# Kernel tuning notes

Hardware: AMD Instinct MI355X
Metric: run time of the kernel (lower is better)

Reference implementation:

```python
import jax, jax.numpy as jnp
import numpy as np
import itertools

B, NM, NS, K, HID, NLAYER, MAXZ, OUT = 64, 32, 32, 3, 64, 4, 100, 1
S = B * NS
NREAL = NM - 2  # real nodes per graph (rest padded)


def setup_inputs() -> dict:
    key = jax.random.key(0)
    ks = jax.random.split(key, 12)
    x = jax.random.randint(ks[0], (B, NM, 1), 0, MAXZ + 1, dtype=jnp.int32)
    subadj = jax.random.uniform(ks[1], (B, NM, NM), dtype=jnp.float32)
    # K distinct node ids per subgraph, all within the real (non-padded) nodes
    subgs = jnp.argsort(jax.random.uniform(ks[2], (S, NREAL)), axis=1)[:, :K].astype(jnp.int32)
    num_node = jnp.full((B,), NREAL, dtype=jnp.int32)
    num_subg = jnp.full((B,), NS, dtype=jnp.int32)
    sc = 0.05
    idemb = jax.random.normal(ks[3], (K + 2, HID), jnp.float32) * sc
    node_emb = jax.random.normal(ks[4], (MAXZ + 1, HID), jnp.float32) * sc
    mlp_W1 = jax.random.normal(ks[5], (NLAYER, HID, HID), jnp.float32) * sc
    mlp_b1 = jnp.zeros((NLAYER, HID), jnp.float32)
    mlp_W2 = jax.random.normal(ks[6], (NLAYER, HID, HID), jnp.float32) * sc
    mlp_b2 = jnp.zeros((NLAYER, HID), jnp.float32)
    mlp_g = jnp.ones((NLAYER, HID), jnp.float32)
    mlp_be = jnp.zeros((NLAYER, HID), jnp.float32)
    set1_W = jax.random.normal(ks[7], (HID, HID), jnp.float32) * sc
    set1_b = jnp.zeros((HID,), jnp.float32)
    set2_W = jax.random.normal(ks[8], (HID, HID), jnp.float32) * sc
    set2_b = jnp.zeros((HID,), jnp.float32)
    out_W = jax.random.normal(ks[9], (HID, OUT), jnp.float32) * sc
    out_b = jnp.zeros((OUT,), jnp.float32)
    return dict(x=x, subadj=subadj, subgs=subgs, num_node=num_node, num_subg=num_subg,
                idemb=idemb, node_emb=node_emb, mlp_W1=mlp_W1, mlp_b1=mlp_b1,
                mlp_W2=mlp_W2, mlp_b2=mlp_b2, mlp_g=mlp_g, mlp_be=mlp_be,
                set1_W=set1_W, set1_b=set1_b, set2_W=set2_W, set2_b=set2_b,
                out_W=out_W, out_b=out_b)


def _layernorm(z, g, b):
    m = z.mean(-1, keepdims=True)
    v = ((z - m) ** 2).mean(-1, keepdims=True)
    return (z - m) / jnp.sqrt(v + 1e-5) * g + b


def _forward(x, subadj, subgs, num_node,
             idemb, node_emb, mlp_W1, mlp_b1, mlp_W2, mlp_b2, mlp_g, mlp_be,
             set1_W, set1_b, set2_W, set2_b, out_W, out_b):
    # allperm: (K, K!) -- matches registered buffer extracttuple(arange(k),k).t()
    allperm = jnp.asarray(np.array(list(itertools.permutations(range(K))), dtype=np.int32).T)
    P = allperm.shape[1]  # K! permutations
    subgbatch = jnp.repeat(jnp.arange(B), NS)                       # (S,) graph id of each subgraph
    null_mask = jnp.arange(NM)[None, :] >= num_node[:, None]        # (B, NM) padded-node mask
    h = node_emb[x[..., 0]]                                         # (B, NM, HID) inmlp embedding
    h = jnp.broadcast_to(h[subgbatch][:, :, None, :], (S, NM, P, HID))  # gather per subgraph, expand perms
    # CSR scatter-assign of permutation id embeddings (all rows full size K, distinct nodes)
    labelbatch = jnp.repeat(jnp.arange(S), K)                       # (S*K,)
    labelnodes = subgs.reshape(-1)                                  # (S*K,)
    nodeidx = jnp.tile(jnp.arange(K), S)                            # position within subgraph
    emb = idemb[allperm[nodeidx]]                                   # (S*K, P, HID)
    h = h.at[labelbatch, labelnodes].multiply(emb)                  # unique (subg,node) pairs
    A = subadj[subgbatch]                                           # (S, NM, NM), float path (d=1 broadcast)
    for l in range(NLAYER):
        m = jnp.einsum('bij,bjpd->bipd', A, h)                      # noindexbmm
        m = jax.nn.relu(m @ mlp_W1[l] + mlp_b1[l])
        m = m @ mlp_W2[l] + mlp_b2[l]
        m = jax.nn.relu(_layernorm(m, mlp_g[l], mlp_be[l]))
        h = h + m
    h = jnp.where(null_mask[subgbatch][:, :, None, None], 0.0, h)   # zero padded nodes
    h = jax.nn.relu(h.mean(axis=2) @ set1_W + set1_b)               # setmlp1 over perm-mean: (S, NM, HID)
    h = jax.nn.relu(h.sum(axis=1) @ set2_W + set2_b)                # setmlp2 over node-sum: (S, HID)
    pooled = jax.ops.segment_max(h, subgbatch, num_segments=B)      # global_max_pool: (B, HID)
    return pooled @ out_W + out_b                                   # (B, OUT)


def reference(x, subadj, subgs, num_node, num_subg,
              idemb, node_emb, mlp_W1, mlp_b1, mlp_W2, mlp_b2, mlp_g, mlp_be,
              set1_W, set1_b, set2_W, set2_b, out_W, out_b):
    return _forward(x, subadj, subgs, num_node,
                    idemb, node_emb, mlp_W1, mlp_b1, mlp_W2, mlp_b2, mlp_g, mlp_be,
                    set1_W, set1_b, set2_W, set2_b, out_W, out_b)
```

## Files before the change

### kernel.cpp

```cpp
#include <hip/hip_runtime.h>
#include <math.h>


#define NBATCH 64
#define NM 32
#define NS 32
#define KSUB 3
#define HID 64
#define NLAYER 4
#define PP 6

#define W1F 0
#define W2F 16384
#define S1F 32768
#define GMAX_BYTE 73728
#define CNT_BYTE  90112
#define S2WT_BYTE 90368

#define SH 68
#define SG 36
#define WBU 2304

typedef _Float16 f16x8 __attribute__((ext_vector_type(8)));
typedef _Float16 f16x2 __attribute__((ext_vector_type(2)));
typedef __fp16 fp16x2 __attribute__((ext_vector_type(2)));
typedef float f32x4 __attribute__((ext_vector_type(4)));

#define MFMA16(a, b, c) __builtin_amdgcn_mfma_f32_16x16x32_f16(a, b, c, 0, 0, 0)

__constant__ int c_perm[KSUB][PP] = {
    {0, 0, 1, 1, 2, 2},
    {1, 2, 0, 2, 0, 1},
    {2, 1, 2, 0, 1, 0}
};

__device__ __forceinline__ unsigned pk2rtz(float a, float b) {
    union { fp16x2 h; unsigned u; } x;
    x.h = __builtin_amdgcn_cvt_pkrtz(a, b);
    return x.u;
}
__device__ __forceinline__ uint2 pk4rtz(float a, float b, float c, float d) {
    return make_uint2(pk2rtz(a, b), pk2rtz(c, d));
}
__device__ __forceinline__ unsigned pkadd(unsigned hu, unsigned yu) {
    union { f16x2 h; unsigned u; } a, b;
    a.u = hu; b.u = yu;
    a.h = a.h + b.h;
    return a.u;
}
__device__ __forceinline__ f16x8 frd(const unsigned short* p) {
    union { struct { uint2 a, b; } u; f16x8 f; } x;
    x.u.a = *(const uint2*)p;
    x.u.b = *(const uint2*)(p + 4);
    return x.f;
}
__device__ __forceinline__ f16x8 gfrd(const unsigned short* p) {
    union { uint4 u; f16x8 f; } x;
    x.u = *(const uint4*)p;
    return x.f;
}

extern "C" __global__ void idmpnn_prep(const float* __restrict__ w1,
                                       const float* __restrict__ w2,
                                       const float* __restrict__ s1w,
                                       const float* __restrict__ s2w,
                                       char* __restrict__ ws)
{
    unsigned short* wsu = (unsigned short*)ws;
    int idx = blockIdx.x * 256 + threadIdx.x;
    float v; int dst;
    if (idx < 16384) {
        int l = idx >> 12, r = idx & 4095, dp = r >> 6, e = r & 63;
        v = w1[l * 4096 + e * 64 + dp];
        dst = W1F + idx;
    } else if (idx < 32768) {
        int k = idx - 16384;
        int l = k >> 12, r = k & 4095, dp = r >> 6, e = r & 63;
        v = w2[l * 4096 + e * 64 + dp];
        dst = W2F + k;
    } else if (idx < 36864) {
        int k = idx - 32768, dp = k >> 6, e = k & 63;
        v = s1w[e * 64 + dp];
        dst = S1F + k;
    } else if (idx < 40960) {
        int k = idx - 36864, dp = k >> 6, e = k & 63;
        ((float*)(ws + S2WT_BYTE))[k] = s2w[e * 64 + dp];
        return;
    } else if (idx < 45056) {
        ((unsigned*)(ws + GMAX_BYTE))[idx - 40960] = 0u;
        return;
    } else if (idx < 45120) {
        ((unsigned*)(ws + CNT_BYTE))[idx - 45056] = 0u;
        return;
    } else return;
    union { _Float16 h; unsigned short u; } cv;
    cv.h = (_Float16)v;
    wsu[dst] = cv.u;
}

extern "C" __global__ void __launch_bounds__(384, 2)
idmpnn_main(const int* __restrict__ xg, const float* __restrict__ subadj,
            const int* __restrict__ subgs, const int* __restrict__ num_node,
            const float* __restrict__ idemb, const float* __restrict__ node_emb,
            const float* __restrict__ b1g, const float* __restrict__ b2g,
            const float* __restrict__ lngm, const float* __restrict__ lnbm,
            const float* __restrict__ s1bm, const float* __restrict__ s2bm,
            const float* __restrict__ outw, const float* __restrict__ outb,
            const unsigned short* __restrict__ wsf, const float* __restrict__ s2wt,
            unsigned* __restrict__ gmax, unsigned* __restrict__ cnt,
            float* __restrict__ out)
{
    __shared__ unsigned short WB[12 * WBU];
    __shared__ float idS[KSUB * 64];
    __shared__ float prm[NLAYER * 4 * 64];
    __shared__ float HSf[2 * HID];

    const int s0 = blockIdx.x * 2;
    const int b = s0 >> 5;
    const int tid = threadIdx.x;
    const int w = tid / 64, lane = tid & 63;
    const int c = lane & 15, q = lane >> 4;

    for (int t = tid; t < NLAYER * 4 * 64; t += 384) {
        int l = t >> 8, r2 = t & 255, set = r2 >> 6, d = r2 & 63;
        const float* src = (set == 0) ? b1g : (set == 1) ? b2g : (set == 2) ? lngm : lnbm;
        prm[t] = src[l * HID + d];
    }
    if (tid < KSUB * 64) idS[tid] = idemb[tid];

    int nd[2][3];
#pragma unroll
    for (int ch = 0; ch < 2; ++ch)
#pragma unroll
        for (int k = 0; k < 3; ++k)
            nd[ch][k] = subgs[(s0 + ch) * KSUB + k];
    const int nn = num_node[b];
    const int zi0 = xg[b * NM + c];
    const int zi1 = xg[b * NM + 16 + c];

    f16x8 adjf[2];
#pragma unroll
    for (int in_ = 0; in_ < 2; ++in_) {
        const float* ap = subadj + (size_t)b * NM * NM + (in_ * 16 + c) * NM + 8 * q;
        float4 f0 = *(const float4*)ap;
        float4 f1 = *(const float4*)(ap + 4);
        union { struct { uint2 a, b; } u; f16x8 f; } x;
        x.u.a = pk4rtz(f0.x, f0.y, f0.z, f0.w);
        x.u.b = pk4rtz(f1.x, f1.y, f1.z, f1.w);
        adjf[in_] = x.f;
    }

    __syncthreads();

    unsigned short* wbc[2] = { WB + (w * 2 + 0) * WBU, WB + (w * 2 + 1) * WBU };
    const int p = w;

    unsigned hpk[2][16];
#pragma unroll
    for (int in_ = 0; in_ < 2; ++in_) {
        int i = in_ * 16 + c;
        int z = in_ ? zi1 : zi0;
        int pid[2];
#pragma unroll
        for (int ch = 0; ch < 2; ++ch)
            pid[ch] = (i == nd[ch][0]) ? c_perm[0][p] : (i == nd[ch][1]) ? c_perm[1][p]
                      : (i == nd[ch][2]) ? c_perm[2][p] : -1;
#pragma unroll
        for (int dm = 0; dm < 4; ++dm) {
            float4 e4 = *(const float4*)(node_emb + (size_t)z * HID + dm * 16 + 4 * q);
#pragma unroll
            for (int ch = 0; ch < 2; ++ch) {
                float4 v = e4;
                if (pid[ch] >= 0) {
                    float4 f4 = *(const float4*)&idS[pid[ch] * 64 + dm * 16 + 4 * q];
                    v.x *= f4.x; v.y *= f4.y; v.z *= f4.z; v.w *= f4.w;
                }
                uint2 u = pk4rtz(v.x, v.y, v.z, v.w);
                hpk[ch][in_ * 8 + dm * 2 + 0] = u.x;
                hpk[ch][in_ * 8 + dm * 2 + 1] = u.y;
            }
        }
    }

#pragma unroll 1
    for (int l = 0; l < NLAYER; ++l) {
#pragma unroll
        for (int ch = 0; ch < 2; ++ch)
#pragma unroll
            for (int in_ = 0; in_ < 2; ++in_)
#pragma unroll
                for (int dm = 0; dm < 4; ++dm)
                    *(uint2*)(wbc[ch] + (in_ * 16 + c) * SH + dm * 16 + 4 * q) =
                        make_uint2(hpk[ch][in_ * 8 + dm * 2], hpk[ch][in_ * 8 + dm * 2 + 1]);

        f16x8 hah[2][2][2];
#pragma unroll
        for (int ch = 0; ch < 2; ++ch)
#pragma unroll
            for (int im = 0; im < 2; ++im)
#pragma unroll
                for (int ks = 0; ks < 2; ++ks)
                    hah[ch][im][ks] = frd(wbc[ch] + (im * 16 + c) * SH + ks * 32 + 8 * q);

#pragma unroll
        for (int jn = 0; jn < 4; ++jn) {
            const unsigned short* wp = wsf + W1F + (l * 64 + jn * 16 + c) * 64;
            f16x8 b0 = gfrd(wp + 8 * q);
            f16x8 b1 = gfrd(wp + 32 + 8 * q);
#pragma unroll
            for (int ch = 0; ch < 2; ++ch) {
                f32x4 g0 = {0.f, 0.f, 0.f, 0.f}, g1 = {0.f, 0.f, 0.f, 0.f};
                g0 = MFMA16(hah[ch][0][0], b0, g0);
                g0 = MFMA16(hah[ch][0][1], b1, g0);
                g1 = MFMA16(hah[ch][1][0], b0, g1);
                g1 = MFMA16(hah[ch][1][1], b1, g1);
                *(uint2*)(wbc[ch] + (jn * 16 + c) * SG + 4 * q)      = pk4rtz(g0[0], g0[1], g0[2], g0[3]);
                *(uint2*)(wbc[ch] + (jn * 16 + c) * SG + 16 + 4 * q) = pk4rtz(g1[0], g1[1], g1[2], g1[3]);
            }
        }

        f16x8 gah[2][4];
#pragma unroll
        for (int ch = 0; ch < 2; ++ch)
#pragma unroll
            for (int dm = 0; dm < 4; ++dm)
                gah[ch][dm] = frd(wbc[ch] + (dm * 16 + c) * SG + 8 * q);

#pragma unroll
        for (int dm = 0; dm < 4; ++dm) {
            float4 b1v = *(const float4*)&prm[(l * 4 + 0) * 64 + dm * 16 + 4 * q];
#pragma unroll
            for (int ch = 0; ch < 2; ++ch) {
                f32x4 t0 = {0.f, 0.f, 0.f, 0.f}, t1 = {0.f, 0.f, 0.f, 0.f};
                t0 = MFMA16(gah[ch][dm], adjf[0], t0);
                t1 = MFMA16(gah[ch][dm], adjf[1], t1);
                *(uint2*)(wbc[ch] + c * SH + dm * 16 + 4 * q) =
                    pk4rtz(fmaxf(t0[0] + b1v.x, 0.f), fmaxf(t0[1] + b1v.y, 0.f),
                           fmaxf(t0[2] + b1v.z, 0.f), fmaxf(t0[3] + b1v.w, 0.f));
                *(uint2*)(wbc[ch] + (16 + c) * SH + dm * 16 + 4 * q) =
                    pk4rtz(fmaxf(t1[0] + b1v.x, 0.f), fmaxf(t1[1] + b1v.y, 0.f),
                           fmaxf(t1[2] + b1v.z, 0.f), fmaxf(t1[3] + b1v.w, 0.f));
            }
        }

        f16x8 tbh[2][2][2];
#pragma unroll
        for (int ch = 0; ch < 2; ++ch)
#pragma unroll
            for (int in_ = 0; in_ < 2; ++in_)
#pragma unroll
                for (int ks = 0; ks < 2; ++ks)
                    tbh[ch][in_][ks] = frd(wbc[ch] + (in_ * 16 + c) * SH + ks * 32 + 8 * q);

#pragma unroll
        for (int in_ = 0; in_ < 2; ++in_) {
            float v[2][16];
            float s1[2] = {0.f, 0.f}, s2[2] = {0.f, 0.f};
#pragma unroll
            for (int dm = 0; dm < 4; ++dm) {
                const unsigned short* wp2 = wsf + W2F + (l * 64 + dm * 16 + c) * 64;
                f16x8 a0 = gfrd(wp2 + 8 * q);
                f16x8 a1 = gfrd(wp2 + 32 + 8 * q);
                float4 b2v = *(const float4*)&prm[(l * 4 + 1) * 64 + dm * 16 + 4 * q];
                const float* bb = (const float*)&b2v;
#pragma unroll
                for (int ch = 0; ch < 2; ++ch) {
                    f32x4 u = {0.f, 0.f, 0.f, 0.f};
                    u = MFMA16(a0, tbh[ch][in_][0], u);
                    u = MFMA16(a1, tbh[ch][in_][1], u);
#pragma unroll
                    for (int r = 0; r < 4; ++r) {
                        float x = u[r] + bb[r];
                        v[ch][dm * 4 + r] = x;
                        s1[ch] += x;
                        s2[ch] += x * x;
                    }
                }
            }
#pragma unroll
            for (int ch = 0; ch < 2; ++ch) {
                float a1 = s1[ch], a2 = s2[ch];
                a1 += __shfl_xor(a1, 16, 64); a1 += __shfl_xor(a1, 32, 64);
                a2 += __shfl_xor(a2, 16, 64); a2 += __shfl_xor(a2, 32, 64);
                float mean = a1 * (1.0f / HID);
                float var  = a2 * (1.0f / HID) - mean * mean;
                float rs   = rsqrtf(var + 1e-5f);
#pragma unroll
                for (int dm = 0; dm < 4; ++dm) {
                    float4 gv4  = *(const float4*)&prm[(l * 4 + 2) * 64 + dm * 16 + 4 * q];
                    float4 bev4 = *(const float4*)&prm[(l * 4 + 3) * 64 + dm * 16 + 4 * q];
                    const float* gp = (const float*)&gv4;
                    const float* bp = (const float*)&bev4;
                    float y0 = fmaxf((v[ch][dm * 4 + 0] - mean) * rs * gp[0] + bp[0], 0.f);
                    float y1 = fmaxf((v[ch][dm * 4 + 1] - mean) * rs * gp[1] + bp[1], 0.f);
                    float y2 = fmaxf((v[ch][dm * 4 + 2] - mean) * rs * gp[2] + bp[2], 0.f);
                    float y3 = fmaxf((v[ch][dm * 4 + 3] - mean) * rs * gp[3] + bp[3], 0.f);
                    int i0 = in_ * 8 + dm * 2;
                    hpk[ch][i0 + 0] = pkadd(hpk[ch][i0 + 0], pk2rtz(y0, y1));
                    hpk[ch][i0 + 1] = pkadd(hpk[ch][i0 + 1], pk2rtz(y2, y3));
                }
            }
        }
    }

#pragma unroll
    for (int ch = 0; ch < 2; ++ch)
#pragma unroll
        for (int in_ = 0; in_ < 2; ++in_)
#pragma unroll
            for (int dm = 0; dm < 4; ++dm)
                *(uint2*)(wbc[ch] + (in_ * 16 + c) * SH + dm * 16 + 4 * q) =
                    make_uint2(hpk[ch][in_ * 8 + dm * 2], hpk[ch][in_ * 8 + dm * 2 + 1]);
    __syncthreads();

    if (w < 2) {
        f16x8 mah[2][2];
#pragma unroll
        for (int im = 0; im < 2; ++im) {
            float sc = ((im * 16 + c) < nn) ? (1.0f / PP) : 0.f;
#pragma unroll
            for (int ks = 0; ks < 2; ++ks) {
                int ro = (im * 16 + c) * SH + ks * 32 + 8 * q;
                float acc8[8];
#pragma unroll
                for (int j = 0; j < 8; ++j) acc8[j] = 0.f;
#pragma unroll
                for (int wv = 0; wv < 6; ++wv) {
                    f16x8 f = frd(WB + (wv * 2 + w) * WBU + ro);
#pragma unroll
                    for (int j = 0; j < 8; ++j) acc8[j] += (float)f[j];
                }
                f16x8 m;
#pragma unroll
                for (int j = 0; j < 8; ++j) m[j] = (_Float16)(acc8[j] * sc);
                mah[im][ks] = m;
            }
        }

        f32x4 hh[2][4];
#pragma unroll
        for (int im = 0; im < 2; ++im)
#pragma unroll
            for (int jn = 0; jn < 4; ++jn) hh[im][jn] = (f32x4){0.f, 0.f, 0.f, 0.f};
#pragma unroll
        for (int jn = 0; jn < 4; ++jn) {
            const unsigned short* sp = wsf + S1F + (jn * 16 + c) * 64;
            f16x8 b0 = gfrd(sp + 8 * q);
            f16x8 b1 = gfrd(sp + 32 + 8 * q);
#pragma unroll
            for (int im = 0; im < 2; ++im) {
                hh[im][jn] = MFMA16(mah[im][0], b0, hh[im][jn]);
                hh[im][jn] = MFMA16(mah[im][1], b1, hh[im][jn]);
            }
        }
#pragma unroll
        for (int jn = 0; jn < 4; ++jn) {
            float sb = s1bm[jn * 16 + c];
            float cs = 0.f;
#pragma unroll
            for (int im = 0; im < 2; ++im)
#pragma unroll
                for (int r = 0; r < 4; ++r)
                    cs += fmaxf(hh[im][jn][r] + sb, 0.f);
            cs += __shfl_xor(cs, 16, 64);
            cs += __shfl_xor(cs, 32, 64);
            if (q == 0) HSf[w * HID + jn * 16 + c] = cs;
        }

        float acc = 0.f;
#pragma unroll
        for (int e4 = 0; e4 < 16; ++e4) {
            float4 wv = *(const float4*)&s2wt[lane * 64 + e4 * 4];
            float4 hv = *(const float4*)&HSf[w * HID + e4 * 4];
            acc += hv.x * wv.x + hv.y * wv.y + hv.z * wv.z + hv.w * wv.w;
        }
        float h2 = fmaxf(acc + s2bm[lane], 0.f);

        atomicMax(&gmax[b * HID + lane], __float_as_uint(h2));
        __threadfence();
        unsigned old = 0;
        if (lane == 0) old = atomicAdd(&cnt[b], 1u);
        old = __shfl(old, 0, 64);
        if (old == NS - 1) {
            __threadfence();
            unsigned mbits = atomicOr(&gmax[b * HID + lane], 0u);
            float v = __uint_as_float(mbits) * outw[lane];
#pragma unroll
            for (int off = 32; off > 0; off >>= 1) v += __shfl_xor(v, off, 64);
            if (lane == 0) out[b] = v + outb[0];
        }
    }
}

extern "C" void kernel_launch(void* const* d_in, const int* in_sizes, int n_in,
                              void* d_out, int out_size, void* d_ws, size_t ws_size,
                              hipStream_t stream)
{
    const int*   xg       = (const int*)d_in[0];
    const float* subadj   = (const float*)d_in[1];
    const int*   subgs    = (const int*)d_in[2];
    const int*   num_node = (const int*)d_in[3];
    const float* idemb    = (const float*)d_in[5];
    const float* node_emb = (const float*)d_in[6];
    const float* w1       = (const float*)d_in[7];
    const float* b1       = (const float*)d_in[8];
    const float* w2       = (const float*)d_in[9];
    const float* b2       = (const float*)d_in[10];
    const float* g        = (const float*)d_in[11];
    const float* be       = (const float*)d_in[12];
    const float* s1w      = (const float*)d_in[13];
    const float* s1b      = (const float*)d_in[14];
    const float* s2w      = (const float*)d_in[15];
    const float* s2b      = (const float*)d_in[16];
    const float* outw     = (const float*)d_in[17];
    const float* outb     = (const float*)d_in[18];

    char* ws = (char*)d_ws;
    unsigned short* wsf = (unsigned short*)ws;
    const float* s2wt = (const float*)(ws + S2WT_BYTE);
    unsigned* gmax = (unsigned*)(ws + GMAX_BYTE);
    unsigned* cnt  = (unsigned*)(ws + CNT_BYTE);

    idmpnn_prep<<<177, 256, 0, stream>>>(w1, w2, s1w, s2w, ws);
    idmpnn_main<<<NBATCH * NS / 2, 384, 0, stream>>>(xg, subadj, subgs, num_node,
                                          idemb, node_emb,
                                          b1, b2, g, be, s1b, s2b, outw, outb,
                                          wsf, s2wt, gmax, cnt, (float*)d_out);
}
```

Measured before the change: 215.8 us.

## Switch to 16x16x16 MFMA so layer chain stays in registers without LDS round-trips

Replaces the 16x16x32 f16 MFMA with the 16x16x16 variant, whose output fragment layout matches its input fragment layout. This lets the per-layer chain (h*W1, adjacency matmul, W2, layernorm) pass fp16-packed results directly between MFMAs in registers, removing the LDS store/reload staging of h, g and t. The cost is twice as many MFMA instructions, each with half the K depth, and higher register pressure from holding more packed intermediates. The per-wave LDS buffer also shrinks because the SG staging area is no longer needed.

```diff
diff --git a/kernel.cpp b/kernel.cpp
--- a/kernel.cpp
+++ b/kernel.cpp
@@ -18,15 +18,14 @@
 #define S2WT_BYTE 90368
 
 #define SH 68
-#define SG 36
-#define WBU 2304
-
-typedef _Float16 f16x8 __attribute__((ext_vector_type(8)));
+#define WBU 2176
+
+typedef _Float16 f16x4 __attribute__((ext_vector_type(4)));
 typedef _Float16 f16x2 __attribute__((ext_vector_type(2)));
 typedef __fp16 fp16x2 __attribute__((ext_vector_type(2)));
 typedef float f32x4 __attribute__((ext_vector_type(4)));
 
-#define MFMA16(a, b, c) __builtin_amdgcn_mfma_f32_16x16x32_f16(a, b, c, 0, 0, 0)
+#define MFMA16(a, b, c) __builtin_amdgcn_mfma_f32_16x16x16f16(a, b, c, 0, 0, 0)
 
 __constant__ int c_perm[KSUB][PP] = {
     {0, 0, 1, 1, 2, 2},
@@ -34,6 +33,8 @@
     {2, 1, 2, 0, 1, 0}
 };
 
+union U2F { uint2 u; f16x4 f; };
+
 __device__ __forceinline__ unsigned pk2rtz(float a, float b) {
     union { fp16x2 h; unsigned u; } x;
     x.h = __builtin_amdgcn_cvt_pkrtz(a, b);
@@ -42,22 +43,19 @@
 __device__ __forceinline__ uint2 pk4rtz(float a, float b, float c, float d) {
     return make_uint2(pk2rtz(a, b), pk2rtz(c, d));
 }
+__device__ __forceinline__ f16x4 fpk4(float a, float b, float c, float d) {
+    U2F x; x.u = pk4rtz(a, b, c, d); return x.f;
+}
+__device__ __forceinline__ f16x4 asf(uint2 u) { U2F x; x.u = u; return x.f; }
 __device__ __forceinline__ unsigned pkadd(unsigned hu, unsigned yu) {
     union { f16x2 h; unsigned u; } a, b;
     a.u = hu; b.u = yu;
     a.h = a.h + b.h;
     return a.u;
 }
-__device__ __forceinline__ f16x8 frd(const unsigned short* p) {
-    union { struct { uint2 a, b; } u; f16x8 f; } x;
-    x.u.a = *(const uint2*)p;
-    x.u.b = *(const uint2*)(p + 4);
-    return x.f;
-}
-__device__ __forceinline__ f16x8 gfrd(const unsigned short* p) {
-    union { uint4 u; f16x8 f; } x;
-    x.u = *(const uint4*)p;
-    return x.f;
+__device__ __forceinline__ float2 upk2(unsigned u) {
+    union { unsigned u; _Float16 h[2]; } x; x.u = u;
+    return make_float2((float)x.h[0], (float)x.h[1]);
 }
 
 extern "C" __global__ void idmpnn_prep(const float* __restrict__ w1,
@@ -138,17 +136,15 @@
     const int zi0 = xg[b * NM + c];
     const int zi1 = xg[b * NM + 16 + c];
 
-    f16x8 adjf[2];
-#pragma unroll
-    for (int in_ = 0; in_ < 2; ++in_) {
-        const float* ap = subadj + (size_t)b * NM * NM + (in_ * 16 + c) * NM + 8 * q;
-        float4 f0 = *(const float4*)ap;
-        float4 f1 = *(const float4*)(ap + 4);
-        union { struct { uint2 a, b; } u; f16x8 f; } x;
-        x.u.a = pk4rtz(f0.x, f0.y, f0.z, f0.w);
-        x.u.b = pk4rtz(f1.x, f1.y, f1.z, f1.w);
-        adjf[in_] = x.f;
-    }
+    uint2 adjb[2][2];
+#pragma unroll
+    for (int in_ = 0; in_ < 2; ++in_)
+#pragma unroll
+        for (int kb = 0; kb < 2; ++kb) {
+            float4 f = *(const float4*)(subadj + (size_t)b * NM * NM
+                                        + (in_ * 16 + c) * NM + kb * 16 + 4 * q);
+            adjb[in_][kb] = pk4rtz(f.x, f.y, f.z, f.w);
+        }
 
     __syncthreads();
 
@@ -184,106 +180,76 @@
 
 #pragma unroll 1
     for (int l = 0; l < NLAYER; ++l) {
-#pragma unroll
-        for (int ch = 0; ch < 2; ++ch)
-#pragma unroll
-            for (int in_ = 0; in_ < 2; ++in_)
-#pragma unroll
-                for (int dm = 0; dm < 4; ++dm)
-                    *(uint2*)(wbc[ch] + (in_ * 16 + c) * SH + dm * 16 + 4 * q) =
-                        make_uint2(hpk[ch][in_ * 8 + dm * 2], hpk[ch][in_ * 8 + dm * 2 + 1]);
-
-        f16x8 hah[2][2][2];
-#pragma unroll
-        for (int ch = 0; ch < 2; ++ch)
-#pragma unroll
-            for (int im = 0; im < 2; ++im)
-#pragma unroll
-                for (int ks = 0; ks < 2; ++ks)
-                    hah[ch][im][ks] = frd(wbc[ch] + (im * 16 + c) * SH + ks * 32 + 8 * q);
-
+        uint2 gpk[2][2][4];
 #pragma unroll
         for (int jn = 0; jn < 4; ++jn) {
-            const unsigned short* wp = wsf + W1F + (l * 64 + jn * 16 + c) * 64;
-            f16x8 b0 = gfrd(wp + 8 * q);
-            f16x8 b1 = gfrd(wp + 32 + 8 * q);
+            uint2 w1f[4];
+#pragma unroll
+            for (int kb = 0; kb < 4; ++kb)
+                w1f[kb] = *(const uint2*)(wsf + W1F + (l * 64 + jn * 16 + c) * 64
+                                          + kb * 16 + 4 * q);
+#pragma unroll
+            for (int ch = 0; ch < 2; ++ch)
+#pragma unroll
+                for (int im = 0; im < 2; ++im) {
+                    f32x4 acc = {0.f, 0.f, 0.f, 0.f};
+#pragma unroll
+                    for (int kb = 0; kb < 4; ++kb)
+                        acc = MFMA16(asf(make_uint2(hpk[ch][im * 8 + kb * 2],
+                                                    hpk[ch][im * 8 + kb * 2 + 1])),
+                                     asf(w1f[kb]), acc);
+                    gpk[ch][im][jn] = pk4rtz(acc[0], acc[1], acc[2], acc[3]);
+                }
+        }
+
+        uint2 tpk[2][4][2];
+#pragma unroll
+        for (int dmA = 0; dmA < 4; ++dmA) {
+            float4 b1v = *(const float4*)&prm[(l * 4 + 0) * 64 + dmA * 16 + 4 * q];
+#pragma unroll
+            for (int ch = 0; ch < 2; ++ch)
+#pragma unroll
+                for (int in_ = 0; in_ < 2; ++in_) {
+                    f32x4 acc = {0.f, 0.f, 0.f, 0.f};
+#pragma unroll
+                    for (int kb = 0; kb < 2; ++kb)
+                        acc = MFMA16(asf(gpk[ch][kb][dmA]), asf(adjb[in_][kb]), acc);
+                    tpk[ch][dmA][in_] = pk4rtz(fmaxf(acc[0] + b1v.x, 0.f),
+                                               fmaxf(acc[1] + b1v.y, 0.f),
+                                               fmaxf(acc[2] + b1v.z, 0.f),
+                                               fmaxf(acc[3] + b1v.w, 0.f));
+                }
+        }
+
+#pragma unroll
+        for (int in_ = 0; in_ < 2; ++in_)
 #pragma unroll
             for (int ch = 0; ch < 2; ++ch) {
-                f32x4 g0 = {0.f, 0.f, 0.f, 0.f}, g1 = {0.f, 0.f, 0.f, 0.f};
-                g0 = MFMA16(hah[ch][0][0], b0, g0);
-                g0 = MFMA16(hah[ch][0][1], b1, g0);
-                g1 = MFMA16(hah[ch][1][0], b0, g1);
-                g1 = MFMA16(hah[ch][1][1], b1, g1);
-                *(uint2*)(wbc[ch] + (jn * 16 + c) * SG + 4 * q)      = pk4rtz(g0[0], g0[1], g0[2], g0[3]);
-                *(uint2*)(wbc[ch] + (jn * 16 + c) * SG + 16 + 4 * q) = pk4rtz(g1[0], g1[1], g1[2], g1[3]);
-            }
-        }
-
-        f16x8 gah[2][4];
-#pragma unroll
-        for (int ch = 0; ch < 2; ++ch)
-#pragma unroll
-            for (int dm = 0; dm < 4; ++dm)
-                gah[ch][dm] = frd(wbc[ch] + (dm * 16 + c) * SG + 8 * q);
-
-#pragma unroll
-        for (int dm = 0; dm < 4; ++dm) {
-            float4 b1v = *(const float4*)&prm[(l * 4 + 0) * 64 + dm * 16 + 4 * q];
-#pragma unroll
-            for (int ch = 0; ch < 2; ++ch) {
-                f32x4 t0 = {0.f, 0.f, 0.f, 0.f}, t1 = {0.f, 0.f, 0.f, 0.f};
-                t0 = MFMA16(gah[ch][dm], adjf[0], t0);
-                t1 = MFMA16(gah[ch][dm], adjf[1], t1);
-                *(uint2*)(wbc[ch] + c * SH + dm * 16 + 4 * q) =
-                    pk4rtz(fmaxf(t0[0] + b1v.x, 0.f), fmaxf(t0[1] + b1v.y, 0.f),
-                           fmaxf(t0[2] + b1v.z, 0.f), fmaxf(t0[3] + b1v.w, 0.f));
-                *(uint2*)(wbc[ch] + (16 + c) * SH + dm * 16 + 4 * q) =
-                    pk4rtz(fmaxf(t1[0] + b1v.x, 0.f), fmaxf(t1[1] + b1v.y, 0.f),
-                           fmaxf(t1[2] + b1v.z, 0.f), fmaxf(t1[3] + b1v.w, 0.f));
-            }
-        }
-
-        f16x8 tbh[2][2][2];
-#pragma unroll
-        for (int ch = 0; ch < 2; ++ch)
-#pragma unroll
-            for (int in_ = 0; in_ < 2; ++in_)
-#pragma unroll
-                for (int ks = 0; ks < 2; ++ks)
-                    tbh[ch][in_][ks] = frd(wbc[ch] + (in_ * 16 + c) * SH + ks * 32 + 8 * q);
-
-#pragma unroll
-        for (int in_ = 0; in_ < 2; ++in_) {
-            float v[2][16];
-            float s1[2] = {0.f, 0.f}, s2[2] = {0.f, 0.f};
-#pragma unroll
-            for (int dm = 0; dm < 4; ++dm) {
-                const unsigned short* wp2 = wsf + W2F + (l * 64 + dm * 16 + c) * 64;
-                f16x8 a0 = gfrd(wp2 + 8 * q);
-                f16x8 a1 = gfrd(wp2 + 32 + 8 * q);
-                float4 b2v = *(const float4*)&prm[(l * 4 + 1) * 64 + dm * 16 + 4 * q];
-                const float* bb = (const float*)&b2v;
-#pragma unroll
-                for (int ch = 0; ch < 2; ++ch) {
-                    f32x4 u = {0.f, 0.f, 0.f, 0.f};
-                    u = MFMA16(a0, tbh[ch][in_][0], u);
-                    u = MFMA16(a1, tbh[ch][in_][1], u);
+                float v[16];
+                float s1 = 0.f, s2 = 0.f;
+#pragma unroll
+                for (int dm = 0; dm < 4; ++dm) {
+                    f32x4 acc = {0.f, 0.f, 0.f, 0.f};
+#pragma unroll
+                    for (int kb = 0; kb < 4; ++kb) {
+                        uint2 w2f = *(const uint2*)(wsf + W2F + (l * 64 + dm * 16 + c) * 64
+                                                    + kb * 16 + 4 * q);
+                        acc = MFMA16(asf(w2f), asf(tpk[ch][kb][in_]), acc);
+                    }
+                    float4 b2v = *(const float4*)&prm[(l * 4 + 1) * 64 + dm * 16 + 4 * q];
+                    const float* bb = (const float*)&b2v;
 #pragma unroll
                     for (int r = 0; r < 4; ++r) {
-                        float x = u[r] + bb[r];
-                        v[ch][dm * 4 + r] = x;
-                        s1[ch] += x;
-                        s2[ch] += x * x;
+                        float x = acc[r] + bb[r];
+                        v[dm * 4 + r] = x;
+                        s1 += x;
+                        s2 += x * x;
                     }
                 }
-            }
-#pragma unroll
-            for (int ch = 0; ch < 2; ++ch) {
-                float a1 = s1[ch], a2 = s2[ch];
-                a1 += __shfl_xor(a1, 16, 64); a1 += __shfl_xor(a1, 32, 64);
-                a2 += __shfl_xor(a2, 16, 64); a2 += __shfl_xor(a2, 32, 64);
-                float mean = a1 * (1.0f / HID);
-                float var  = a2 * (1.0f / HID) - mean * mean;
+                s1 += __shfl_xor(s1, 16, 64); s1 += __shfl_xor(s1, 32, 64);
+                s2 += __shfl_xor(s2, 16, 64); s2 += __shfl_xor(s2, 32, 64);
+                float mean = s1 * (1.0f / HID);
+                float var  = s2 * (1.0f / HID) - mean * mean;
                 float rs   = rsqrtf(var + 1e-5f);
 #pragma unroll
                 for (int dm = 0; dm < 4; ++dm) {
@@ -291,16 +257,15 @@
                     float4 bev4 = *(const float4*)&prm[(l * 4 + 3) * 64 + dm * 16 + 4 * q];
                     const float* gp = (const float*)&gv4;
                     const float* bp = (const float*)&bev4;
-                    float y0 = fmaxf((v[ch][dm * 4 + 0] - mean) * rs * gp[0] + bp[0], 0.f);
-                    float y1 = fmaxf((v[ch][dm * 4 + 1] - mean) * rs * gp[1] + bp[1], 0.f);
-                    float y2 = fmaxf((v[ch][dm * 4 + 2] - mean) * rs * gp[2] + bp[2], 0.f);
-                    float y3 = fmaxf((v[ch][dm * 4 + 3] - mean) * rs * gp[3] + bp[3], 0.f);
+                    float y0 = fmaxf((v[dm * 4 + 0] - mean) * rs * gp[0] + bp[0], 0.f);
+                    float y1 = fmaxf((v[dm * 4 + 1] - mean) * rs * gp[1] + bp[1], 0.f);
+                    float y2 = fmaxf((v[dm * 4 + 2] - mean) * rs * gp[2] + bp[2], 0.f);
+                    float y3 = fmaxf((v[dm * 4 + 3] - mean) * rs * gp[3] + bp[3], 0.f);
                     int i0 = in_ * 8 + dm * 2;
                     hpk[ch][i0 + 0] = pkadd(hpk[ch][i0 + 0], pk2rtz(y0, y1));
                     hpk[ch][i0 + 1] = pkadd(hpk[ch][i0 + 1], pk2rtz(y2, y3));
                 }
             }
-        }
     }
 
 #pragma unroll
@@ -314,26 +279,21 @@
     __syncthreads();
 
     if (w < 2) {
-        f16x8 mah[2][2];
+        f16x4 mah[2][4];
 #pragma unroll
         for (int im = 0; im < 2; ++im) {
             float sc = ((im * 16 + c) < nn) ? (1.0f / PP) : 0.f;
 #pragma unroll
-            for (int ks = 0; ks < 2; ++ks) {
-                int ro = (im * 16 + c) * SH + ks * 32 + 8 * q;
-                float acc8[8];
-#pragma unroll
-                for (int j = 0; j < 8; ++j) acc8[j] = 0.f;
+            for (int kb = 0; kb < 4; ++kb) {
+                int ro = (im * 16 + c) * SH + kb * 16 + 4 * q;
+                float a0 = 0.f, a1 = 0.f, a2 = 0.f, a3 = 0.f;
 #pragma unroll
                 for (int wv = 0; wv < 6; ++wv) {
-                    f16x8 f = frd(WB + (wv * 2 + w) * WBU + ro);
-#pragma unroll
-                    for (int j = 0; j < 8; ++j) acc8[j] += (float)f[j];
-                }
-                f16x8 m;
-#pragma unroll
-                for (int j = 0; j < 8; ++j) m[j] = (_Float16)(acc8[j] * sc);
-                mah[im][ks] = m;
+                    uint2 t = *(const uint2*)(WB + (wv * 2 + w) * WBU + ro);
+                    float2 p0 = upk2(t.x), p1 = upk2(t.y);
+                    a0 += p0.x; a1 += p0.y; a2 += p1.x; a3 += p1.y;
+                }
+                mah[im][kb] = fpk4(a0 * sc, a1 * sc, a2 * sc, a3 * sc);
             }
         }
 
@@ -343,16 +303,14 @@
 #pragma unroll
             for (int jn = 0; jn < 4; ++jn) hh[im][jn] = (f32x4){0.f, 0.f, 0.f, 0.f};
 #pragma unroll
-        for (int jn = 0; jn < 4; ++jn) {
-            const unsigned short* sp = wsf + S1F + (jn * 16 + c) * 64;
-            f16x8 b0 = gfrd(sp + 8 * q);
-            f16x8 b1 = gfrd(sp + 32 + 8 * q);
-#pragma unroll
-            for (int im = 0; im < 2; ++im) {
-                hh[im][jn] = MFMA16(mah[im][0], b0, hh[im][jn]);
-                hh[im][jn] = MFMA16(mah[im][1], b1, hh[im][jn]);
+        for (int jn = 0; jn < 4; ++jn)
+#pragma unroll
+            for (int kb = 0; kb < 4; ++kb) {
+                uint2 s1f = *(const uint2*)(wsf + S1F + (jn * 16 + c) * 64 + kb * 16 + 4 * q);
+#pragma unroll
+                for (int im = 0; im < 2; ++im)
+                    hh[im][jn] = MFMA16(mah[im][kb], asf(s1f), hh[im][jn]);
             }
-        }
 #pragma unroll
         for (int jn = 0; jn < 4; ++jn) {
             float sb = s1bm[jn * 16 + c];
```

Measured after the change: 240.1 us. +11.3%, slower.

## Remap work to one subgraph per block with each wave handling two permutations

Applied to the files above, without the earlier changes.

The main kernel now launches one block per subgraph with 3 waves instead of one block per two subgraphs with 6 waves. Each wave processes two permutations of the same subgraph rather than one permutation of two subgraphs, and the shared buffer shrinks by half. The aim is more, smaller blocks for better CU load balance and occupancy. The residual add also changes from a packed half-precision add to a float add followed by repacking, which improves accuracy but costs extra conversions. The tail phase now runs on a single wave, and the per-graph atomic counter now receives 32 increments, one per block, which still matches the NS-1 completion check.

```diff
diff --git a/kernel.cpp b/kernel.cpp
--- a/kernel.cpp
+++ b/kernel.cpp
@@ -9,6 +9,7 @@
 #define HID 64
 #define NLAYER 4
 #define PP 6
+#define STOT (NBATCH * NS)
 
 #define W1F 0
 #define W2F 16384
@@ -22,7 +23,6 @@
 #define WBU 2304
 
 typedef _Float16 f16x8 __attribute__((ext_vector_type(8)));
-typedef _Float16 f16x2 __attribute__((ext_vector_type(2)));
 typedef __fp16 fp16x2 __attribute__((ext_vector_type(2)));
 typedef float f32x4 __attribute__((ext_vector_type(4)));
 
@@ -42,12 +42,6 @@
 __device__ __forceinline__ uint2 pk4rtz(float a, float b, float c, float d) {
     return make_uint2(pk2rtz(a, b), pk2rtz(c, d));
 }
-__device__ __forceinline__ unsigned pkadd(unsigned hu, unsigned yu) {
-    union { f16x2 h; unsigned u; } a, b;
-    a.u = hu; b.u = yu;
-    a.h = a.h + b.h;
-    return a.u;
-}
 __device__ __forceinline__ f16x8 frd(const unsigned short* p) {
     union { struct { uint2 a, b; } u; f16x8 f; } x;
     x.u.a = *(const uint2*)p;
@@ -58,6 +52,10 @@
     union { uint4 u; f16x8 f; } x;
     x.u = *(const uint4*)p;
     return x.f;
+}
+__device__ __forceinline__ float2 upk2(unsigned u) {
+    union { unsigned u; _Float16 h[2]; } x; x.u = u;
+    return make_float2((float)x.h[0], (float)x.h[1]);
 }
 
 extern "C" __global__ void idmpnn_prep(const float* __restrict__ w1,
@@ -98,7 +96,7 @@
     wsu[dst] = cv.u;
 }
 
-extern "C" __global__ void __launch_bounds__(384, 2)
+extern "C" __global__ void __launch_bounds__(192, 3)
 idmpnn_main(const int* __restrict__ xg, const float* __restrict__ subadj,
             const int* __restrict__ subgs, const int* __restrict__ num_node,
             const float* __restrict__ idemb, const float* __restrict__ node_emb,
@@ -110,30 +108,26 @@
             unsigned* __restrict__ gmax, unsigned* __restrict__ cnt,
             float* __restrict__ out)
 {
-    __shared__ unsigned short WB[12 * WBU];
+    __shared__ unsigned short WB[6 * WBU];
     __shared__ float idS[KSUB * 64];
     __shared__ float prm[NLAYER * 4 * 64];
-    __shared__ float HSf[2 * HID];
-
-    const int s0 = blockIdx.x * 2;
-    const int b = s0 >> 5;
+    __shared__ float HSf[HID];
+
+    const int s = blockIdx.x, b = s >> 5;
     const int tid = threadIdx.x;
     const int w = tid / 64, lane = tid & 63;
     const int c = lane & 15, q = lane >> 4;
 
-    for (int t = tid; t < NLAYER * 4 * 64; t += 384) {
+    for (int t = tid; t < NLAYER * 4 * 64; t += 192) {
         int l = t >> 8, r2 = t & 255, set = r2 >> 6, d = r2 & 63;
         const float* src = (set == 0) ? b1g : (set == 1) ? b2g : (set == 2) ? lngm : lnbm;
         prm[t] = src[l * HID + d];
     }
     if (tid < KSUB * 64) idS[tid] = idemb[tid];
 
-    int nd[2][3];
-#pragma unroll
-    for (int ch = 0; ch < 2; ++ch)
-#pragma unroll
-        for (int k = 0; k < 3; ++k)
-            nd[ch][k] = subgs[(s0 + ch) * KSUB + k];
+    const int nd0 = subgs[s * KSUB + 0];
+    const int nd1 = subgs[s * KSUB + 1];
+    const int nd2 = subgs[s * KSUB + 2];
     const int nn = num_node[b];
     const int zi0 = xg[b * NM + c];
     const int zi1 = xg[b * NM + 16 + c];
@@ -153,7 +147,6 @@
     __syncthreads();
 
     unsigned short* wbc[2] = { WB + (w * 2 + 0) * WBU, WB + (w * 2 + 1) * WBU };
-    const int p = w;
 
     unsigned hpk[2][16];
 #pragma unroll
@@ -162,9 +155,11 @@
         int z = in_ ? zi1 : zi0;
         int pid[2];
 #pragma unroll
-        for (int ch = 0; ch < 2; ++ch)
-            pid[ch] = (i == nd[ch][0]) ? c_perm[0][p] : (i == nd[ch][1]) ? c_perm[1][p]
-                      : (i == nd[ch][2]) ? c_perm[2][p] : -1;
+        for (int ch = 0; ch < 2; ++ch) {
+            int p = w * 2 + ch;
+            pid[ch] = (i == nd0) ? c_perm[0][p] : (i == nd1) ? c_perm[1][p]
+                      : (i == nd2) ? c_perm[2][p] : -1;
+        }
 #pragma unroll
         for (int dm = 0; dm < 4; ++dm) {
             float4 e4 = *(const float4*)(node_emb + (size_t)z * HID + dm * 16 + 4 * q);
@@ -296,8 +291,10 @@
                     float y2 = fmaxf((v[ch][dm * 4 + 2] - mean) * rs * gp[2] + bp[2], 0.f);
                     float y3 = fmaxf((v[ch][dm * 4 + 3] - mean) * rs * gp[3] + bp[3], 0.f);
                     int i0 = in_ * 8 + dm * 2;
-                    hpk[ch][i0 + 0] = pkadd(hpk[ch][i0 + 0], pk2rtz(y0, y1));
-                    hpk[ch][i0 + 1] = pkadd(hpk[ch][i0 + 1], pk2rtz(y2, y3));
+                    float2 h0 = upk2(hpk[ch][i0 + 0]);
+                    float2 h1 = upk2(hpk[ch][i0 + 1]);
+                    hpk[ch][i0 + 0] = pk2rtz(h0.x + y0, h0.y + y1);
+                    hpk[ch][i0 + 1] = pk2rtz(h1.x + y2, h1.y + y3);
                 }
             }
         }
@@ -313,7 +310,7 @@
                     make_uint2(hpk[ch][in_ * 8 + dm * 2], hpk[ch][in_ * 8 + dm * 2 + 1]);
     __syncthreads();
 
-    if (w < 2) {
+    if (w == 0) {
         f16x8 mah[2][2];
 #pragma unroll
         for (int im = 0; im < 2; ++im) {
@@ -325,8 +322,8 @@
 #pragma unroll
                 for (int j = 0; j < 8; ++j) acc8[j] = 0.f;
 #pragma unroll
-                for (int wv = 0; wv < 6; ++wv) {
-                    f16x8 f = frd(WB + (wv * 2 + w) * WBU + ro);
+                for (int pv = 0; pv < 6; ++pv) {
+                    f16x8 f = frd(WB + pv * WBU + ro);
 #pragma unroll
                     for (int j = 0; j < 8; ++j) acc8[j] += (float)f[j];
                 }
@@ -364,14 +361,14 @@
                     cs += fmaxf(hh[im][jn][r] + sb, 0.f);
             cs += __shfl_xor(cs, 16, 64);
             cs += __shfl_xor(cs, 32, 64);
-            if (q == 0) HSf[w * HID + jn * 16 + c] = cs;
+            if (q == 0) HSf[jn * 16 + c] = cs;
         }
 
         float acc = 0.f;
 #pragma unroll
         for (int e4 = 0; e4 < 16; ++e4) {
             float4 wv = *(const float4*)&s2wt[lane * 64 + e4 * 4];
-            float4 hv = *(const float4*)&HSf[w * HID + e4 * 4];
+            float4 hv = *(const float4*)&HSf[e4 * 4];
             acc += hv.x * wv.x + hv.y * wv.y + hv.z * wv.z + hv.w * wv.w;
         }
         float h2 = fmaxf(acc + s2bm[lane], 0.f);
@@ -422,7 +419,7 @@
     unsigned* cnt  = (unsigned*)(ws + CNT_BYTE);
 
     idmpnn_prep<<<177, 256, 0, stream>>>(w1, w2, s1w, s2w, ws);
-    idmpnn_main<<<NBATCH * NS / 2, 384, 0, stream>>>(xg, subadj, subgs, num_node,
+    idmpnn_main<<<STOT, 192, 0, stream>>>(xg, subadj, subgs, num_node,
                                           idemb, node_emb,
                                           b1, b2, g, be, s1b, s2b, outw, outb,
                                           wsf, s2wt, gmax, cnt, (float*)d_out);
```

New measurement: 233.4 us. 8.1% more time.
